# Performance work log

Measured on AMD Instinct MI355X. Metric: run time of the kernel, lower is better.

## Reference

```python
import jax, jax.numpy as jnp
import numpy as np

B, N, D = 8, 2048, 512

def setup_inputs() -> dict:
    key = jax.random.key(0)
    k1, k2, k3, k4, k5 = jax.random.split(key, 5)
    s = 1.0 / np.sqrt(D)
    return {
        "x": jax.random.normal(k1, (B, N, D), dtype=jnp.float32),
        "w_qkv": jax.random.normal(k2, (D, 3 * D), dtype=jnp.float32) * s,
        "b_qkv": jax.random.normal(k3, (3 * D,), dtype=jnp.float32) * 0.01,
        "w_fc": jax.random.normal(k4, (D, D), dtype=jnp.float32) * s,
        "b_fc": jax.random.normal(k5, (D,), dtype=jnp.float32) * 0.01,
    }

def reference(x, w_qkv, b_qkv, w_fc, b_fc):
    scale = 1.0 / (x.shape[-1] ** 0.5)
    qkv = x @ w_qkv + b_qkv                      # [B, N, 3D]
    q, k, v = jnp.split(qkv, 3, axis=-1)         # each [B, N, D]
    attn = jnp.einsum("bnd,bmd->bnm", q, k) * scale
    attn = jax.nn.softmax(attn, axis=-1)
    out = jnp.einsum("bnm,bmd->bnd", attn, v)
    return out @ w_fc + b_fc + x
```

## Files before the change

### kernel.cpp

```cpp
#include <hip/hip_runtime.h>
#include <stdint.h>

typedef unsigned short u16;
typedef unsigned int u32;
typedef __attribute__((ext_vector_type(8))) short short8;
typedef __attribute__((ext_vector_type(4))) float f32x4;
typedef __attribute__((ext_vector_type(8))) unsigned short u16x8;
typedef __attribute__((ext_vector_type(4))) float float4_t;

__device__ __forceinline__ float b2f(u16 u) { return __uint_as_float(((u32)u) << 16); }
__device__ __forceinline__ u16 f2b(float f) {
  u32 u = __float_as_uint(f);
  u += 0x7fffu + ((u >> 16) & 1u);
  return (u16)(u >> 16);
}

typedef const __attribute__((address_space(1))) void* gas_t;
typedef __attribute__((address_space(3))) void* las_t;
__device__ __forceinline__ void gl_lds16(const void* g, void* l) {
  __builtin_amdgcn_global_load_lds((gas_t)(uintptr_t)g, (las_t)(u32)(uintptr_t)l, 16, 0, 0);
}
__device__ __forceinline__ void barrier_pin() {
  __builtin_amdgcn_sched_barrier(0);
  __builtin_amdgcn_s_barrier();
  __builtin_amdgcn_sched_barrier(0);
}

__global__ __launch_bounds__(256) void cvt_f2b_kernel(const float* __restrict__ src,
                                                      u16* __restrict__ dst, long n) {
  long i = ((long)blockIdx.x * 256 + threadIdx.x) * 8;
  if (i >= n) return;
  float4_t v0 = *(const float4_t*)(src + i);
  float4_t v1 = *(const float4_t*)(src + i + 4);
  u16x8 o;
#pragma unroll
  for (int j = 0; j < 4; ++j) { o[j] = f2b(v0[j]); o[4 + j] = f2b(v1[j]); }
  *(u16x8*)(dst + i) = o;
}

__global__ __launch_bounds__(256) void tr_cvt(const float* __restrict__ src,
                                              u16* __restrict__ dst, int R, int C) {
  __shared__ float t[32][33];
  const int bx = blockIdx.x * 32;
  const int by = blockIdx.y * 32;
  const int tx = threadIdx.x & 31, ty = threadIdx.x >> 5;
#pragma unroll
  for (int i = 0; i < 32; i += 8)
    t[ty + i][tx] = src[(long)(by + ty + i) * C + bx + tx];
  __syncthreads();
#pragma unroll
  for (int i = 0; i < 32; i += 8)
    dst[(long)(bx + ty + i) * R + by + tx] = f2b(t[tx][ty + i]);
}

__global__ __launch_bounds__(256) void tr_v(const u16* __restrict__ qkv, u16* __restrict__ vt) {
  __shared__ u16 t[32][33];
  const int b = blockIdx.z;
  const int r0 = blockIdx.x * 32;
  const int d0 = blockIdx.y * 32;
  const int tx = threadIdx.x & 31, ty = threadIdx.x >> 5;
#pragma unroll
  for (int i = 0; i < 32; i += 8)
    t[ty + i][tx] = qkv[((long)b * 2048 + r0 + ty + i) * 1536 + 1024 + d0 + tx];
  __syncthreads();
#pragma unroll
  for (int i = 0; i < 32; i += 8)
    vt[((long)b * 512 + d0 + ty + i) * 2048 + r0 + tx] = t[tx][ty + i];
}

template <int NREP, bool OUT_F32, bool BIAS, bool RES>
__global__ __launch_bounds__(512, 1)
void gemm256(const u16* __restrict__ A, const u16* __restrict__ Bt, void* __restrict__ Cv,
             const float* __restrict__ bias, const float* __restrict__ res,
             int K, int lda, int ldb, int ldc,
             long aStride, long bStride, long cStride, float alpha) {
  __shared__ u16 As[2][256 * 64];
  __shared__ u16 Bs[2][NREP * 64 * 64];
  const int tid = threadIdx.x;
  const int wid = tid >> 6, lane = tid & 63;
  const int wr = wid >> 2, wc = wid & 3;
  const int lr = lane & 15, lg = lane >> 4;

  const int gx = gridDim.x, gy = gridDim.y;
  int id = (blockIdx.z * gy + blockIdx.y) * gx + blockIdx.x;
  const int nwg = gx * gy * gridDim.z;
  id = (id & 7) * (nwg >> 3) + (id >> 3);
  const int bxi = id % gx;
  const int t2 = id / gx;
  const int byi = t2 % gy;
  const long z = t2 / gy;

  A += z * aStride;
  Bt += z * bStride;
  const int by = byi * 256;
  const int bx = bxi * (NREP * 64);

  f32x4 acc[8][NREP] = {};

  const int w8l = wid * 8 + (lane >> 3);
  const int scol_src = ((lane & 7) ^ (lane >> 3)) * 8;
  const int scol_lin = (lane & 7) * 8;
  const int nT = K >> 6;

  auto stage_A = [&](int h, int kt) {
    const int bb = kt & 1;
    const long kc = (long)kt * 64 + scol_src;
#pragma unroll
    for (int r = 0; r < 2; ++r) {
      const int row = h * 128 + r * 64 + w8l;
      gl_lds16(A + (long)(by + row) * lda + kc, &As[bb][row * 64 + scol_lin]);
    }
  };
  auto stage_B = [&](int h, int kt) {
    const int bb = kt & 1;
    const long kc = (long)kt * 64 + scol_src;
#pragma unroll
    for (int r = 0; r < 2; ++r) {
      const int row = h * 128 + r * 64 + w8l;
      gl_lds16(Bt + (long)(bx + row) * ldb + kc, &Bs[bb][row * 64 + scol_lin]);
    }
  };

  const int sx = lane & 7;
  auto do_phase = [&](int bb, int q) {
    if constexpr (NREP == 4) {
      const int mh = q >> 1, nh = q & 1;
      short8 a[4][2], b[2][2];
#pragma unroll
      for (int mi = 0; mi < 4; ++mi)
#pragma unroll
        for (int ks = 0; ks < 2; ++ks)
          a[mi][ks] = *(const short8*)&As[bb][(mh * 128 + wr * 64 + mi * 16 + lr) * 64 +
                                             (((ks * 4 + lg) ^ sx) * 8)];
#pragma unroll
      for (int ni = 0; ni < 2; ++ni)
#pragma unroll
        for (int ks = 0; ks < 2; ++ks)
          b[ni][ks] = *(const short8*)&Bs[bb][(nh * 128 + wc * 32 + ni * 16 + lr) * 64 +
                                             (((ks * 4 + lg) ^ sx) * 8)];
      __builtin_amdgcn_s_setprio(1);
#pragma unroll
      for (int mi = 0; mi < 4; ++mi)
#pragma unroll
        for (int ni = 0; ni < 2; ++ni)
#pragma unroll
          for (int ks = 0; ks < 2; ++ks)
            acc[mh * 4 + mi][nh * 2 + ni] = __builtin_amdgcn_mfma_f32_16x16x32_bf16(
                a[mi][ks], b[ni][ks], acc[mh * 4 + mi][nh * 2 + ni], 0, 0, 0);
      __builtin_amdgcn_s_setprio(0);
    } else {
      const int mh = q >> 1, kh = q & 1;
      short8 a[4], b[2];
#pragma unroll
      for (int mi = 0; mi < 4; ++mi)
        a[mi] = *(const short8*)&As[bb][(mh * 128 + wr * 64 + mi * 16 + lr) * 64 +
                                        (((kh * 4 + lg) ^ sx) * 8)];
#pragma unroll
      for (int ni = 0; ni < 2; ++ni)
        b[ni] = *(const short8*)&Bs[bb][(wc * 32 + ni * 16 + lr) * 64 +
                                        (((kh * 4 + lg) ^ sx) * 8)];
      __builtin_amdgcn_s_setprio(1);
#pragma unroll
      for (int mi = 0; mi < 4; ++mi)
#pragma unroll
        for (int ni = 0; ni < 2; ++ni)
          acc[mh * 4 + mi][ni] = __builtin_amdgcn_mfma_f32_16x16x32_bf16(
              a[mi], b[ni], acc[mh * 4 + mi][ni], 0, 0, 0);
      __builtin_amdgcn_s_setprio(0);
    }
  };

  stage_A(0, 0); stage_A(1, 0); stage_B(0, 0);
  if constexpr (NREP == 4) stage_B(1, 0);
  stage_A(0, 1);
  asm volatile("s_waitcnt vmcnt(2)" ::: "memory");
  barrier_pin();

  for (int T = 0; T < nT; T += 2) {
    const bool more = (T + 2) < nT;
    stage_A(1, T + 1); stage_B(0, T + 1);
    do_phase(0, 0);
    barrier_pin();
    if constexpr (NREP == 4) stage_B(1, T + 1);
    do_phase(0, 1);
    barrier_pin();
    if (more) stage_A(0, T + 2);
    do_phase(0, 2);
    barrier_pin();
    do_phase(0, 3);
    if (more) asm volatile("s_waitcnt vmcnt(2)" ::: "memory");
    else      asm volatile("s_waitcnt vmcnt(0)" ::: "memory");
    barrier_pin();
    if (more) stage_A(1, T + 2);
    do_phase(1, 0);
    barrier_pin();
    if (more) stage_B(0, T + 2);
    do_phase(1, 1);
    barrier_pin();
    if constexpr (NREP == 4) { if (more) stage_B(1, T + 2); }
    do_phase(1, 2);
    barrier_pin();
    if (more) stage_A(0, T + 3);
    do_phase(1, 3);
    if (more) asm volatile("s_waitcnt vmcnt(2)" ::: "memory");
    barrier_pin();
  }

  if constexpr (OUT_F32) {
    float* C = (float*)Cv + z * cStride;
#pragma unroll
    for (int mi = 0; mi < 8; ++mi)
#pragma unroll
      for (int ni = 0; ni < NREP; ++ni)
#pragma unroll
        for (int j = 0; j < 4; ++j) {
          const long row = by + (mi >> 2) * 128 + wr * 64 + (mi & 3) * 16 + lg * 4 + j;
          const int col = (NREP == 4)
                              ? bx + (ni >> 1) * 128 + wc * 32 + (ni & 1) * 16 + lr
                              : bx + wc * 32 + ni * 16 + lr;
          float v = acc[mi][ni][j] * alpha;
          if (BIAS) v += bias[col];
          if (RES) v += res[row * (long)ldc + col];
          C[row * (long)ldc + col] = v;
        }
  } else {
    u16* C = (u16*)Cv + z * cStride;
#pragma unroll
    for (int mi = 0; mi < 8; ++mi)
#pragma unroll
      for (int ni = 0; ni < NREP; ++ni)
#pragma unroll
        for (int j = 0; j < 4; ++j) {
          const long row = by + (mi >> 2) * 128 + wr * 64 + (mi & 3) * 16 + lg * 4 + j;
          const int col = (NREP == 4)
                              ? bx + (ni >> 1) * 128 + wc * 32 + (ni & 1) * 16 + lr
                              : bx + wc * 32 + ni * 16 + lr;
          float v = acc[mi][ni][j] * alpha;
          if (BIAS) v += bias[col];
          C[row * (long)ldc + col] = f2b(v);
        }
  }
}

__global__ __launch_bounds__(256) void softmax_rows(u16* __restrict__ S) {
  const long row = blockIdx.x;
  u16* p = S + row * 2048;
  const int tid = threadIdx.x;
  const int wid = tid >> 6, lane = tid & 63;
  u16x8 v = ((const u16x8*)p)[tid];
  float f[8];
#pragma unroll
  for (int j = 0; j < 8; ++j) f[j] = b2f(v[j]);
  float m = f[0];
#pragma unroll
  for (int j = 1; j < 8; ++j) m = fmaxf(m, f[j]);
#pragma unroll
  for (int off = 32; off; off >>= 1) m = fmaxf(m, __shfl_xor(m, off));
  __shared__ float rmax[4], rsum[4];
  if (lane == 0) rmax[wid] = m;
  __syncthreads();
  m = fmaxf(fmaxf(rmax[0], rmax[1]), fmaxf(rmax[2], rmax[3]));
  float s = 0.f;
#pragma unroll
  for (int j = 0; j < 8; ++j) { f[j] = __expf(f[j] - m); s += f[j]; }
#pragma unroll
  for (int off = 32; off; off >>= 1) s += __shfl_xor(s, off);
  if (lane == 0) rsum[wid] = s;
  __syncthreads();
  s = rsum[0] + rsum[1] + rsum[2] + rsum[3];
  const float inv = 1.0f / s;
  u16x8 o;
#pragma unroll
  for (int j = 0; j < 8; ++j) o[j] = f2b(f[j] * inv);
  ((u16x8*)p)[tid] = o;
}

extern "C" void kernel_launch(void* const* d_in, const int* in_sizes, int n_in,
                              void* d_out, int out_size, void* d_ws, size_t ws_size,
                              hipStream_t stream) {
  const float* x = (const float*)d_in[0];
  const float* w_qkv = (const float*)d_in[1];
  const float* b_qkv = (const float*)d_in[2];
  const float* w_fc = (const float*)d_in[3];
  const float* b_fc = (const float*)d_in[4];
  float* out = (float*)d_out;

  char* ws = (char*)d_ws;
  const long MT = 16384;
  u16* xb = (u16*)(ws);
  u16* wqkvT = (u16*)(ws + 16777216);
  u16* wfcT = (u16*)(ws + 18350080);
  u16* qkv = (u16*)(ws + 18874368);
  u16* vt = (u16*)(ws + 69206016);
  u16* S = (u16*)(ws + 85983232);
  u16* attn = xb;

  cvt_f2b_kernel<<<4096, 256, 0, stream>>>(x, xb, MT * 512);
  tr_cvt<<<dim3(48, 16), 256, 0, stream>>>(w_qkv, wqkvT, 512, 1536);
  tr_cvt<<<dim3(16, 16), 256, 0, stream>>>(w_fc, wfcT, 512, 512);

  gemm256<2, false, true, false><<<dim3(12, 64, 1), 512, 0, stream>>>(
      xb, wqkvT, qkv, b_qkv, nullptr, 512, 512, 512, 1536, 0, 0, 0, 1.0f);

  tr_v<<<dim3(64, 16, 8), 256, 0, stream>>>(qkv, vt);

  gemm256<4, false, false, false><<<dim3(8, 8, 8), 512, 0, stream>>>(
      qkv, qkv + 512, S, nullptr, nullptr, 512, 1536, 1536, 2048,
      (long)2048 * 1536, (long)2048 * 1536, (long)2048 * 2048, 0.04419417382415922f);

  softmax_rows<<<16384, 256, 0, stream>>>(S);

  gemm256<2, false, false, false><<<dim3(4, 8, 8), 512, 0, stream>>>(
      S, vt, attn, nullptr, nullptr, 2048, 2048, 2048, 512,
      (long)2048 * 2048, (long)512 * 2048, (long)2048 * 512, 1.0f);

  gemm256<2, true, true, true><<<dim3(4, 64, 1), 512, 0, stream>>>(
      attn, wfcT, out, b_fc, x, 512, 512, 512, 512, 0, 0, 0, 1.0f);
}
```

Measured before the change: 189.1 us.

## Hold B fragments in registers and halve the number of pipeline phases

```diff
diff --git a/kernel.cpp b/kernel.cpp
--- a/kernel.cpp
+++ b/kernel.cpp
@@ -96,11 +96,13 @@
   const int bx = bxi * (NREP * 64);
 
   f32x4 acc[8][NREP] = {};
+  short8 bh[NREP][2];
 
   const int w8l = wid * 8 + (lane >> 3);
   const int scol_src = ((lane & 7) ^ (lane >> 3)) * 8;
   const int scol_lin = (lane & 7) * 8;
   const int nT = K >> 6;
+  const int sx = lane & 7;
 
   auto stage_A = [&](int h, int kt) {
     const int bb = kt & 1;
@@ -111,97 +113,70 @@
       gl_lds16(A + (long)(by + row) * lda + kc, &As[bb][row * 64 + scol_lin]);
     }
   };
-  auto stage_B = [&](int h, int kt) {
+  auto stage_Bf = [&](int kt) {
     const int bb = kt & 1;
     const long kc = (long)kt * 64 + scol_src;
 #pragma unroll
-    for (int r = 0; r < 2; ++r) {
-      const int row = h * 128 + r * 64 + w8l;
+    for (int r = 0; r < NREP; ++r) {
+      const int row = r * 64 + w8l;
       gl_lds16(Bt + (long)(bx + row) * ldb + kc, &Bs[bb][row * 64 + scol_lin]);
     }
   };
 
-  const int sx = lane & 7;
-  auto do_phase = [&](int bb, int q) {
-    if constexpr (NREP == 4) {
-      const int mh = q >> 1, nh = q & 1;
-      short8 a[4][2], b[2][2];
-#pragma unroll
-      for (int mi = 0; mi < 4; ++mi)
+  auto read_B = [&](int bb) {
+#pragma unroll
+    for (int n = 0; n < NREP; ++n) {
+      const int brow = (NREP == 4) ? ((n >> 1) * 128 + wc * 32 + (n & 1) * 16 + lr)
+                                   : (wc * 32 + n * 16 + lr);
+#pragma unroll
+      for (int ks = 0; ks < 2; ++ks)
+        bh[n][ks] = *(const short8*)&Bs[bb][brow * 64 + (((ks * 4 + lg) ^ sx) * 8)];
+    }
+  };
+  auto half_mfma = [&](int bb, int mh) {
+    short8 a[4][2];
+#pragma unroll
+    for (int mi = 0; mi < 4; ++mi)
+#pragma unroll
+      for (int ks = 0; ks < 2; ++ks)
+        a[mi][ks] = *(const short8*)&As[bb][(mh * 128 + wr * 64 + mi * 16 + lr) * 64 +
+                                            (((ks * 4 + lg) ^ sx) * 8)];
+    __builtin_amdgcn_s_setprio(1);
+#pragma unroll
+    for (int mi = 0; mi < 4; ++mi)
+#pragma unroll
+      for (int n = 0; n < NREP; ++n)
 #pragma unroll
         for (int ks = 0; ks < 2; ++ks)
-          a[mi][ks] = *(const short8*)&As[bb][(mh * 128 + wr * 64 + mi * 16 + lr) * 64 +
-                                             (((ks * 4 + lg) ^ sx) * 8)];
-#pragma unroll
-      for (int ni = 0; ni < 2; ++ni)
-#pragma unroll
-        for (int ks = 0; ks < 2; ++ks)
-          b[ni][ks] = *(const short8*)&Bs[bb][(nh * 128 + wc * 32 + ni * 16 + lr) * 64 +
-                                             (((ks * 4 + lg) ^ sx) * 8)];
-      __builtin_amdgcn_s_setprio(1);
-#pragma unroll
-      for (int mi = 0; mi < 4; ++mi)
-#pragma unroll
-        for (int ni = 0; ni < 2; ++ni)
-#pragma unroll
-          for (int ks = 0; ks < 2; ++ks)
-            acc[mh * 4 + mi][nh * 2 + ni] = __builtin_amdgcn_mfma_f32_16x16x32_bf16(
-                a[mi][ks], b[ni][ks], acc[mh * 4 + mi][nh * 2 + ni], 0, 0, 0);
-      __builtin_amdgcn_s_setprio(0);
-    } else {
-      const int mh = q >> 1, kh = q & 1;
-      short8 a[4], b[2];
-#pragma unroll
-      for (int mi = 0; mi < 4; ++mi)
-        a[mi] = *(const short8*)&As[bb][(mh * 128 + wr * 64 + mi * 16 + lr) * 64 +
-                                        (((kh * 4 + lg) ^ sx) * 8)];
-#pragma unroll
-      for (int ni = 0; ni < 2; ++ni)
-        b[ni] = *(const short8*)&Bs[bb][(wc * 32 + ni * 16 + lr) * 64 +
-                                        (((kh * 4 + lg) ^ sx) * 8)];
-      __builtin_amdgcn_s_setprio(1);
-#pragma unroll
-      for (int mi = 0; mi < 4; ++mi)
-#pragma unroll
-        for (int ni = 0; ni < 2; ++ni)
-          acc[mh * 4 + mi][ni] = __builtin_amdgcn_mfma_f32_16x16x32_bf16(
-              a[mi], b[ni], acc[mh * 4 + mi][ni], 0, 0, 0);
-      __builtin_amdgcn_s_setprio(0);
-    }
-  };
-
-  stage_A(0, 0); stage_A(1, 0); stage_B(0, 0);
-  if constexpr (NREP == 4) stage_B(1, 0);
+          acc[mh * 4 + mi][n] = __builtin_amdgcn_mfma_f32_16x16x32_bf16(
+              a[mi][ks], bh[n][ks], acc[mh * 4 + mi][n], 0, 0, 0);
+    __builtin_amdgcn_s_setprio(0);
+  };
+
+  stage_A(0, 0); stage_A(1, 0); stage_Bf(0);
   stage_A(0, 1);
   asm volatile("s_waitcnt vmcnt(2)" ::: "memory");
   barrier_pin();
 
   for (int T = 0; T < nT; T += 2) {
     const bool more = (T + 2) < nT;
-    stage_A(1, T + 1); stage_B(0, T + 1);
-    do_phase(0, 0);
-    barrier_pin();
-    if constexpr (NREP == 4) stage_B(1, T + 1);
-    do_phase(0, 1);
-    barrier_pin();
-    if (more) stage_A(0, T + 2);
-    do_phase(0, 2);
-    barrier_pin();
-    do_phase(0, 3);
-    if (more) asm volatile("s_waitcnt vmcnt(2)" ::: "memory");
-    else      asm volatile("s_waitcnt vmcnt(0)" ::: "memory");
+    stage_A(1, T + 1); stage_Bf(T + 1);
+    read_B(0); half_mfma(0, 0);
+    barrier_pin();
+    if (more) { stage_A(0, T + 2); stage_Bf(T + 2); }
+    half_mfma(0, 1);
+    if (more) {
+      if constexpr (NREP == 4) asm volatile("s_waitcnt vmcnt(6)" ::: "memory");
+      else                     asm volatile("s_waitcnt vmcnt(4)" ::: "memory");
+    } else {
+      asm volatile("s_waitcnt vmcnt(0)" ::: "memory");
+    }
     barrier_pin();
     if (more) stage_A(1, T + 2);
-    do_phase(1, 0);
-    barrier_pin();
-    if (more) stage_B(0, T + 2);
-    do_phase(1, 1);
-    barrier_pin();
-    if constexpr (NREP == 4) { if (more) stage_B(1, T + 2); }
-    do_phase(1, 2);
+    read_B(1); half_mfma(1, 0);
     barrier_pin();
     if (more) stage_A(0, T + 3);
-    do_phase(1, 3);
+    half_mfma(1, 1);
     if (more) asm volatile("s_waitcnt vmcnt(2)" ::: "memory");
     barrier_pin();
   }
```

Measured after the change: 184.4 us. 2.5% less time.
